# Kernel optimization log

Measured on AMD Instinct MI355X. Metric: run time of the kernel, lower is better.

The kernel has to match this reference:

```python
import jax, jax.numpy as jnp
import numpy as np

B, S, D_H, D_L, K, K_H, W = 4, 4096, 1024, 256, 64, 4, 9


def setup_inputs() -> dict:
    key = jax.random.key(0)
    ks = jax.random.split(key, 6)
    return {
        "inputs": jax.random.normal(ks[0], (B, S, D_H), jnp.float32),
        "W1": jax.random.normal(ks[1], (D_H, D_L), jnp.float32) * 0.02,
        "b1": jnp.zeros((D_L,), jnp.float32),
        "RME": jax.random.normal(ks[2], (D_L, K), jnp.float32),
        "K2": jax.random.normal(ks[3], (K_H, D_L, D_L), jnp.float32) * 0.02,
        "b2": jnp.zeros((D_L,), jnp.float32),
        "Wu": jax.random.normal(ks[4], (D_L, D_H), jnp.float32) * 0.02,
        "bu": jnp.zeros((D_H,), jnp.float32),
        "gamma": jnp.ones((D_H,), jnp.float32),
        "beta": jnp.zeros((D_H,), jnp.float32),
    }


def _memory_reorg(act, RMVs, k_h):
    # act: [B,S,d_l], RMVs: [B,S,k]
    R = jnp.transpose(RMVs, (0, 2, 1))  # [B,k,S]
    h_vars = jnp.mean((R - jnp.mean(R, axis=-1, keepdims=True)) ** 2, axis=-1)  # [B,k]
    top = jnp.argsort(-h_vars, axis=-1)[:, :k_h]                   # [B,k_h]
    h_max = jnp.take_along_axis(R, top[:, :, None], axis=1)        # [B,k_h,S]
    perm = jnp.argsort(h_max, axis=-1)                             # [B,k_h,S] permutation indices
    g = jnp.take_along_axis(act[:, None], perm[..., None], axis=2) # [B,k_h,S,d_l]
    return jnp.transpose(g, (0, 2, 1, 3))                          # [B,S,k_h,d_l]


def reference(inputs, W1, b1, RME, K2, b2, Wu, bu, gamma, beta):
    # DOWN_PROJECTION_1
    q = jax.nn.relu(jnp.einsum('bsh,hd->bsd', inputs, W1) + b1)    # [B,S,d_l]
    # RANDOM_PROJECTION
    RMVs = jnp.einsum('bsd,dk->bsk', q, RME)                       # [B,S,k]
    # Memory reorganization (variance-based argsort permutations)
    qp = _memory_reorg(q, RMVs, K_H)                               # [B,S,k_h,d_l]
    # DOWN_PROJECTION_2
    q2 = jax.nn.relu(jnp.einsum('bskd,kde->bse', qp, K2) + b2)     # [B,S,d_l]
    # Sliding-window key construction (edge windows replicated)
    half = (W - 1) // 2
    widx = jnp.arange(S - W + 1)[:, None] + jnp.arange(W)[None, :]  # [S-W+1, W]
    win = q2[:, widx]                                               # [B,S-W+1,W,d_l]
    first = jnp.broadcast_to(q2[:, None, :W], (B, half, W, D_L))
    last = jnp.broadcast_to(q2[:, None, S - W:], (B, half, W, D_L))
    keyt = jnp.concatenate([first, win, last], axis=1)              # [B,S,W,d_l]
    # Windowed attention
    f = jnp.sqrt(jnp.float32(D_L))
    scores = jax.nn.softmax(jnp.einsum('bsd,bswd->bsw', q2, keyt) / f, axis=-1)  # [B,S,W]
    # UP_PROJECTION on keys -> values
    val = jax.nn.relu(jnp.einsum('bswd,dh->bswh', keyt, Wu) + bu)   # [B,S,W,d_h]
    out = jnp.einsum('bswh,bsw->bsh', val, scores)                  # [B,S,d_h]
    # LayerNorm (keras default epsilon=1e-3) on residual
    x = out + inputs
    mu = jnp.mean(x, axis=-1, keepdims=True)
    var = jnp.mean((x - mu) ** 2, axis=-1, keepdims=True)
    return gamma * (x - mu) * jax.lax.rsqrt(var + 1e-3) + beta
```

## Files before the change

### kernel.cpp

```cpp
#include <hip/hip_runtime.h>

#define B_  4
#define S_  4096
#define DH  1024
#define DL  256
#define KK  64
#define KH  4
#define WW  9

typedef unsigned short ushort_t;
typedef _Float16 f16;
typedef _Float16 f16x8 __attribute__((ext_vector_type(8)));
typedef float  f32x4  __attribute__((ext_vector_type(4)));

__device__ __forceinline__ void gld_lds16(const void* g, void* lds_uniform_base) {
    __builtin_amdgcn_global_load_lds(
        (const __attribute__((address_space(1))) unsigned int*)g,
        (__attribute__((address_space(3))) unsigned int*)lds_uniform_base,
        16, 0, 0);
}

template<bool AFP32, bool GATHER, int OUTMODE>
__global__ __launch_bounds__(256)
void mfma_gemm2(const float* __restrict__ Af,
                const ushort_t* __restrict__ Ah, const ushort_t* __restrict__ Al,
                const ushort_t* __restrict__ Bh, const ushort_t* __restrict__ Bl,
                const float* __restrict__ bias, float* __restrict__ C,
                ushort_t* __restrict__ Ch, ushort_t* __restrict__ Cl,
                const int* __restrict__ gidx, int K, int N, int nbx)
{
    __shared__ __align__(16) ushort_t Abuf[64 * 64 * 2];
    __shared__ __align__(16) ushort_t Bsh[128 * 64];
    __shared__ __align__(16) ushort_t Bsl[128 * 64];

    const int tid = threadIdx.x;
    const int w = tid >> 6, l = tid & 63;
    const int wm = w >> 1, wn = w & 1;
    const int lr = l & 15, lk = l >> 4;
    const int cpx = gridDim.x >> 3;
    const int orig = (blockIdx.x & 7) * cpx + (blockIdx.x >> 3);
    const int m0 = (orig / nbx) * 64, n0 = (orig % nbx) * 128;

    f32x4 acc0[2][4] = {};
    f32x4 acc1[2][4] = {};

    for (int k0 = 0; k0 < K; k0 += 64) {
        if (AFP32) {
            float* Asf = (float*)Abuf;
            #pragma unroll
            for (int it = 0; it < 4; ++it) {
                const int c = it * 256 + tid;
                const int r = c >> 4, cc = c & 15;
                const int cs = cc ^ ((r & 7) << 1);
                const float* src = Af + (size_t)(m0 + r) * K + k0 + cs * 4;
                gld_lds16(src, &Asf[(size_t)c * 4]);
            }
        } else {
            ushort_t* Ash = Abuf;
            ushort_t* Asl = Abuf + 64 * 64;
            #pragma unroll
            for (int it = 0; it < 2; ++it) {
                const int c = it * 256 + tid;
                const int r = c >> 3, kp = c & 7;
                const int kl = kp ^ (r & 7);
                size_t off;
                if (GATHER) {
                    const int rg = gidx[(m0 + r) * KH + (k0 >> 8)];
                    off = (size_t)rg * DL + (k0 & (DL - 1)) + kl * 8;
                } else {
                    off = (size_t)(m0 + r) * K + k0 + kl * 8;
                }
                gld_lds16(Ah + off, &Ash[(size_t)c * 8]);
                gld_lds16(Al + off, &Asl[(size_t)c * 8]);
            }
        }
        #pragma unroll
        for (int it = 0; it < 4; ++it) {
            const int c = it * 256 + tid;
            const int r = c >> 3, kp = c & 7;
            const int kl = kp ^ (r & 7);
            const size_t off = (size_t)(n0 + r) * K + k0 + kl * 8;
            gld_lds16(Bh + off, &Bsh[(size_t)c * 8]);
            gld_lds16(Bl + off, &Bsl[(size_t)c * 8]);
        }
        __syncthreads();

        #pragma unroll
        for (int ks = 0; ks < 2; ++ks) {
            f16x8 ah[2], al[2];
            #pragma unroll
            for (int mf = 0; mf < 2; ++mf) {
                const int row = wm * 32 + mf * 16 + lr;
                const int kb  = ks * 4 + lk;
                if (AFP32) {
                    const float* Asf = (const float*)Abuf;
                    const int fo = row * 64 + ((kb ^ (row & 7)) << 3);
                    const f32x4 lo = *(const f32x4*)&Asf[fo];
                    const f32x4 hi = *(const f32x4*)&Asf[fo + 4];
                    const float xs[8] = {lo[0], lo[1], lo[2], lo[3],
                                         hi[0], hi[1], hi[2], hi[3]};
                    #pragma unroll
                    for (int e = 0; e < 8; ++e) {
                        const f16 h = (f16)xs[e];
                        const f16 lv = (f16)((xs[e] - (float)h) * 2048.0f);
                        ah[mf][e] = h;
                        al[mf][e] = lv;
                    }
                } else {
                    const ushort_t* Ash = Abuf;
                    const ushort_t* Asl = Abuf + 64 * 64;
                    const int o = row * 64 + ((kb ^ (row & 7)) << 3);
                    ah[mf] = *(const f16x8*)&Ash[o];
                    al[mf] = *(const f16x8*)&Asl[o];
                }
            }
            #pragma unroll
            for (int nf = 0; nf < 4; ++nf) {
                const int row = wn * 64 + nf * 16 + lr;
                const int kb  = ks * 4 + lk;
                const int o   = row * 64 + ((kb ^ (row & 7)) << 3);
                const f16x8 bh = *(const f16x8*)&Bsh[o];
                const f16x8 bl = *(const f16x8*)&Bsl[o];
                #pragma unroll
                for (int mf = 0; mf < 2; ++mf) {
                    acc0[mf][nf] = __builtin_amdgcn_mfma_f32_16x16x32_f16(
                        ah[mf], bh, acc0[mf][nf], 0, 0, 0);
                    acc1[mf][nf] = __builtin_amdgcn_mfma_f32_16x16x32_f16(
                        ah[mf], bl, acc1[mf][nf], 0, 0, 0);
                    acc1[mf][nf] = __builtin_amdgcn_mfma_f32_16x16x32_f16(
                        al[mf], bh, acc1[mf][nf], 0, 0, 0);
                }
            }
        }
        __syncthreads();
    }

    float bv[4];
    #pragma unroll
    for (int nf = 0; nf < 4; ++nf)
        bv[nf] = bias[n0 + wn * 64 + nf * 16 + lr];
    #pragma unroll
    for (int mf = 0; mf < 2; ++mf)
        #pragma unroll
        for (int nf = 0; nf < 4; ++nf)
            #pragma unroll
            for (int r = 0; r < 4; ++r) {
                const int m = m0 + wm * 32 + mf * 16 + lk * 4 + r;
                const int n = n0 + wn * 64 + nf * 16 + lr;
                float x = acc0[mf][nf][r] + acc1[mf][nf][r] * (1.0f / 2048.0f) + bv[nf];
                x = fmaxf(x, 0.f);
                C[(size_t)m * N + n] = x;
                if (OUTMODE == 1) {
                    const f16 h = (f16)x;
                    const f16 lo = (f16)((x - (float)h) * 2048.0f);
                    Ch[(size_t)m * N + n] = __builtin_bit_cast(ushort_t, h);
                    Cl[(size_t)m * N + n] = __builtin_bit_cast(ushort_t, lo);
                }
            }
}

__global__ __launch_bounds__(512)
void mfma_gemm_big(const ushort_t* __restrict__ Ah, const ushort_t* __restrict__ Al,
                   const ushort_t* __restrict__ Bh, const ushort_t* __restrict__ Bl,
                   const float* __restrict__ bias, ushort_t* __restrict__ Ch,
                   int K, int N, int nbx)
{
    __shared__ __align__(16) ushort_t Ash[128 * 64];
    __shared__ __align__(16) ushort_t Asl[128 * 64];
    __shared__ __align__(16) ushort_t Bsh[128 * 64];
    __shared__ __align__(16) ushort_t Bsl[128 * 64];

    const int tid = threadIdx.x;
    const int w = tid >> 6, l = tid & 63;
    const int wm = w >> 1, wn = w & 1;
    const int lr = l & 15, lk = l >> 4;
    const int cpx = gridDim.x >> 3;
    const int orig = (blockIdx.x & 7) * cpx + (blockIdx.x >> 3);
    const int m0 = (orig / nbx) * 128, n0 = (orig % nbx) * 128;

    f32x4 acc0[2][4] = {};
    f32x4 acc1[2][4] = {};

    for (int k0 = 0; k0 < K; k0 += 64) {
        #pragma unroll
        for (int it = 0; it < 2; ++it) {
            const int c = it * 512 + tid;
            const int r = c >> 3, kp = c & 7;
            const int kl = kp ^ (r & 7);
            const size_t offA = (size_t)(m0 + r) * K + k0 + kl * 8;
            const size_t offB = (size_t)(n0 + r) * K + k0 + kl * 8;
            gld_lds16(Ah + offA, &Ash[(size_t)c * 8]);
            gld_lds16(Al + offA, &Asl[(size_t)c * 8]);
            gld_lds16(Bh + offB, &Bsh[(size_t)c * 8]);
            gld_lds16(Bl + offB, &Bsl[(size_t)c * 8]);
        }
        __syncthreads();

        #pragma unroll
        for (int ks = 0; ks < 2; ++ks) {
            f16x8 ah[2], al[2];
            #pragma unroll
            for (int mf = 0; mf < 2; ++mf) {
                const int row = wm * 32 + mf * 16 + lr;
                const int kb  = ks * 4 + lk;
                const int o   = row * 64 + ((kb ^ (row & 7)) << 3);
                ah[mf] = *(const f16x8*)&Ash[o];
                al[mf] = *(const f16x8*)&Asl[o];
            }
            #pragma unroll
            for (int nf = 0; nf < 4; ++nf) {
                const int row = wn * 64 + nf * 16 + lr;
                const int kb  = ks * 4 + lk;
                const int o   = row * 64 + ((kb ^ (row & 7)) << 3);
                const f16x8 bh = *(const f16x8*)&Bsh[o];
                const f16x8 bl = *(const f16x8*)&Bsl[o];
                #pragma unroll
                for (int mf = 0; mf < 2; ++mf) {
                    acc0[mf][nf] = __builtin_amdgcn_mfma_f32_16x16x32_f16(
                        ah[mf], bh, acc0[mf][nf], 0, 0, 0);
                    acc1[mf][nf] = __builtin_amdgcn_mfma_f32_16x16x32_f16(
                        ah[mf], bl, acc1[mf][nf], 0, 0, 0);
                    acc1[mf][nf] = __builtin_amdgcn_mfma_f32_16x16x32_f16(
                        al[mf], bh, acc1[mf][nf], 0, 0, 0);
                }
            }
        }
        __syncthreads();
    }

    float bv[4];
    #pragma unroll
    for (int nf = 0; nf < 4; ++nf)
        bv[nf] = bias[n0 + wn * 64 + nf * 16 + lr];
    #pragma unroll
    for (int mf = 0; mf < 2; ++mf)
        #pragma unroll
        for (int nf = 0; nf < 4; ++nf)
            #pragma unroll
            for (int r = 0; r < 4; ++r) {
                const int m = m0 + wm * 32 + mf * 16 + lk * 4 + r;
                const int n = n0 + wn * 64 + nf * 16 + lr;
                float x = acc0[mf][nf][r] + acc1[mf][nf][r] * (1.0f / 2048.0f) + bv[nf];
                x = fmaxf(x, 0.f);
                const f16 hcv = (f16)x;
                Ch[(size_t)m * N + n] = __builtin_bit_cast(ushort_t, hcv);
            }
}

__global__ __launch_bounds__(256)
void tsplit2_kernel(const float* __restrict__ in, ushort_t* __restrict__ t0,
                    ushort_t* __restrict__ t1, int K, int N)
{
    __shared__ float tile[32][33];
    const int t = threadIdx.x;
    const int bk = blockIdx.x * 32, bn = blockIdx.y * 32;
    const int c = t & 31, rb = t >> 5;
    #pragma unroll
    for (int i = 0; i < 4; ++i) {
        const int r = rb + i * 8;
        tile[r][c] = in[(size_t)(bk + r) * N + bn + c];
    }
    __syncthreads();
    #pragma unroll
    for (int i = 0; i < 4; ++i) {
        const int rr = rb + i * 8;
        const float x = tile[c][rr];
        const f16 hv = (f16)x;
        const f16 lv = (f16)((x - (float)hv) * 2048.0f);
        const size_t o = (size_t)(bn + rr) * K + bk + c;
        t0[o] = __builtin_bit_cast(ushort_t, hv);
        t1[o] = __builtin_bit_cast(ushort_t, lv);
    }
}

__global__ __launch_bounds__(256)
void gemm_trans_kernel(const float* __restrict__ A, const float* __restrict__ Bm,
                       float* __restrict__ C, int M, int KA, int N)
{
    constexpr int BK = 16;
    __shared__ float Asb[BK][64 + 4];
    __shared__ float Bsb[BK][64 + 4];
    const int tid = threadIdx.x;
    const int tx = tid & 15, ty = tid >> 4;
    const int m0 = blockIdx.y * 64, n0 = blockIdx.x * 64;

    float acc[4][4] = {};
    const int lr = tid >> 2, lc = (tid & 3) << 2;
    const int kr = tid >> 4, nc = (tid & 15) << 2;

    for (int k0 = 0; k0 < KA; k0 += BK) {
        const float4 a4 = *reinterpret_cast<const float4*>(A + (size_t)(m0 + lr) * KA + k0 + lc);
        const float4 b4 = *reinterpret_cast<const float4*>(Bm + (size_t)(k0 + kr) * N + n0 + nc);
        Asb[lc + 0][lr] = a4.x; Asb[lc + 1][lr] = a4.y;
        Asb[lc + 2][lr] = a4.z; Asb[lc + 3][lr] = a4.w;
        *reinterpret_cast<float4*>(&Bsb[kr][nc]) = b4;
        __syncthreads();
        #pragma unroll
        for (int kk = 0; kk < BK; ++kk) {
            const float4 av = *reinterpret_cast<const float4*>(&Asb[kk][ty << 2]);
            const float4 bv = *reinterpret_cast<const float4*>(&Bsb[kk][tx << 2]);
            const float a[4] = {av.x, av.y, av.z, av.w};
            const float b[4] = {bv.x, bv.y, bv.z, bv.w};
            #pragma unroll
            for (int i = 0; i < 4; ++i)
                #pragma unroll
                for (int j = 0; j < 4; ++j)
                    acc[i][j] = fmaf(a[i], b[j], acc[i][j]);
        }
        __syncthreads();
    }
    #pragma unroll
    for (int i = 0; i < 4; ++i) {
        const int m = m0 + (ty << 2) + i;
        const int b = m >> 12, s = m & (S_ - 1);
        #pragma unroll
        for (int j = 0; j < 4; ++j) {
            const int n = n0 + (tx << 2) + j;
            C[(size_t)(b * N + n) * S_ + s] = acc[i][j];
        }
    }
}

__global__ __launch_bounds__(256)
void var_kernel(const float* __restrict__ rmvT, float* __restrict__ hvars)
{
    const int bk = blockIdx.x;
    const float* src = rmvT + (size_t)bk * S_;
    float s1 = 0.f, s2 = 0.f;
    for (int t = threadIdx.x; t < S_; t += 256) {
        const float v = src[t];
        s1 += v; s2 += v * v;
    }
    #pragma unroll
    for (int off = 32; off; off >>= 1) {
        s1 += __shfl_xor(s1, off);
        s2 += __shfl_xor(s2, off);
    }
    __shared__ float r1[4], r2[4];
    const int wave = threadIdx.x >> 6, lane = threadIdx.x & 63;
    if (lane == 0) { r1[wave] = s1; r2[wave] = s2; }
    __syncthreads();
    if (threadIdx.x == 0) {
        const float t1 = r1[0] + r1[1] + r1[2] + r1[3];
        const float t2 = r2[0] + r2[1] + r2[2] + r2[3];
        const float mu = t1 / (float)S_;
        hvars[bk] = t2 / (float)S_ - mu * mu;
    }
}

__global__ void topk_kernel(const float* __restrict__ hvars, int* __restrict__ topidx)
{
    const int b = threadIdx.x;
    if (b >= B_) return;
    float v[KK];
    for (int k = 0; k < KK; ++k) v[k] = hvars[b * KK + k];
    for (int i = 0; i < KH; ++i) {
        int best = 0; float bv = -3.4e38f;
        for (int k = 0; k < KK; ++k)
            if (v[k] > bv) { bv = v[k]; best = k; }
        topidx[b * KH + i] = best;
        v[best] = -3.4e38f;
    }
}

__global__ __launch_bounds__(256)
void rank_kernel(const float* __restrict__ rmvT, const int* __restrict__ topidx,
                 int* __restrict__ gidx)
{
    const int bi = blockIdx.x;
    const int b = bi >> 2, ih = bi & 3;
    const int k = topidx[b * KH + ih];
    const float* src = rmvT + (size_t)(b * KK + k) * S_;
    __shared__ __align__(16) unsigned long long keys[S_];
    __shared__ int partial[4][64];
    for (int t = threadIdx.x; t < S_; t += 256) {
        const unsigned bits = __builtin_bit_cast(unsigned, src[t]);
        const unsigned u = (bits & 0x80000000u) ? ~bits : (bits | 0x80000000u);
        keys[t] = ((unsigned long long)u << 12) | (unsigned)t;
    }
    __syncthreads();

    const int il = threadIdx.x & 63;
    const int chunk = threadIdx.x >> 6;
    const int i = blockIdx.y * 64 + il;
    const unsigned long long ki = keys[i];

    int cnt = 0;
    const int jbase = chunk << 10;
    #pragma unroll 8
    for (int jj = 0; jj < 1024; jj += 2) {
        const ulonglong2 k2 = *reinterpret_cast<const ulonglong2*>(&keys[jbase + jj]);
        cnt += (int)(k2.x < ki);
        cnt += (int)(k2.y < ki);
    }
    partial[chunk][il] = cnt;
    __syncthreads();
    if (threadIdx.x < 64) {
        const int rank = partial[0][threadIdx.x] + partial[1][threadIdx.x]
                       + partial[2][threadIdx.x] + partial[3][threadIdx.x];
        const int ii = blockIdx.y * 64 + threadIdx.x;
        gidx[((b << 12) + rank) * KH + ih] = (b << 12) + ii;
    }
}

__global__ __launch_bounds__(256)
void final_kernel(const ushort_t* __restrict__ vh, const float* __restrict__ q2,
                  const float* __restrict__ inputs, const float* __restrict__ gamma,
                  const float* __restrict__ beta, float* __restrict__ out)
{
    const int bid = blockIdx.x;
    const int m0 = (((bid & 7) << 9) | (bid >> 3)) << 2;
    const int wave = threadIdx.x >> 6, lane = threadIdx.x & 63;
    const int m = m0 + wave;
    const int s = m & (S_ - 1), b = m >> 12;
    const int jb = (s < 4) ? 0 : (s >= S_ - 4 ? S_ - WW : s - 4);

    const ushort_t* vb = vh + (size_t)(b * S_ + jb) * DH;
    const float* inp = inputs + (size_t)m * DH;
    f16x8 varr[2][WW];
    float4 iv[2][2];
    #pragma unroll
    for (int c = 0; c < 2; ++c) {
        const int h = (c << 9) + (lane << 3);
        #pragma unroll
        for (int w = 0; w < WW; ++w)
            varr[c][w] = *reinterpret_cast<const f16x8*>(vb + (size_t)w * DH + h);
        iv[c][0] = *reinterpret_cast<const float4*>(inp + h);
        iv[c][1] = *reinterpret_cast<const float4*>(inp + h + 4);
    }

    const float4 qv = *reinterpret_cast<const float4*>(q2 + (size_t)m * DL + (lane << 2));
    const float* kbase = q2 + (size_t)(b * S_ + jb) * DL;
    float sc[WW];
    #pragma unroll
    for (int w = 0; w < WW; ++w) {
        const float4 kv = *reinterpret_cast<const float4*>(kbase + w * DL + (lane << 2));
        float d = qv.x * kv.x + qv.y * kv.y + qv.z * kv.z + qv.w * kv.w;
        #pragma unroll
        for (int off = 32; off; off >>= 1) d += __shfl_xor(d, off);
        sc[w] = d * 0.0625f;
    }
    float mx = sc[0];
    #pragma unroll
    for (int w = 1; w < WW; ++w) mx = fmaxf(mx, sc[w]);
    float wgt[WW]; float sum = 0.f;
    #pragma unroll
    for (int w = 0; w < WW; ++w) { wgt[w] = __expf(sc[w] - mx); sum += wgt[w]; }
    const float inv = 1.f / sum;
    #pragma unroll
    for (int w = 0; w < WW; ++w) wgt[w] *= inv;

    float x[2][8];
    float s1 = 0.f, s2 = 0.f;
    #pragma unroll
    for (int c = 0; c < 2; ++c) {
        float acc[8] = {};
        #pragma unroll
        for (int w = 0; w < WW; ++w) {
            const f16x8 vv = varr[c][w];
            #pragma unroll
            for (int e = 0; e < 8; ++e)
                acc[e] = fmaf(wgt[w], (float)vv[e], acc[e]);
        }
        #pragma unroll
        for (int e = 0; e < 8; ++e) {
            const float ivv = (e < 4) ? (&iv[c][0].x)[e] : (&iv[c][1].x)[e - 4];
            acc[e] += ivv;
            x[c][e] = acc[e];
            s1 += acc[e];
            s2 += acc[e] * acc[e];
        }
    }

    #pragma unroll
    for (int off = 32; off; off >>= 1) {
        s1 += __shfl_xor(s1, off);
        s2 += __shfl_xor(s2, off);
    }
    const float mu = s1 / (float)DH;
    const float rs = rsqrtf(s2 / (float)DH - mu * mu + 0.001f);

    #pragma unroll
    for (int c = 0; c < 2; ++c) {
        const int h = (c << 9) + (lane << 3);
        #pragma unroll
        for (int half = 0; half < 2; ++half) {
            const float4 g  = *reinterpret_cast<const float4*>(gamma + h + half * 4);
            const float4 bt = *reinterpret_cast<const float4*>(beta + h + half * 4);
            float4 o;
            o.x = g.x * (x[c][half * 4 + 0] - mu) * rs + bt.x;
            o.y = g.y * (x[c][half * 4 + 1] - mu) * rs + bt.y;
            o.z = g.z * (x[c][half * 4 + 2] - mu) * rs + bt.z;
            o.w = g.w * (x[c][half * 4 + 3] - mu) * rs + bt.w;
            *reinterpret_cast<float4*>(out + (size_t)m * DH + h + half * 4) = o;
        }
    }
}

extern "C" void kernel_launch(void* const* d_in, const int* in_sizes, int n_in,
                              void* d_out, int out_size, void* d_ws, size_t ws_size,
                              hipStream_t stream)
{
    (void)in_sizes; (void)n_in; (void)out_size; (void)ws_size;
    const float* inputs = (const float*)d_in[0];
    const float* W1     = (const float*)d_in[1];
    const float* b1     = (const float*)d_in[2];
    const float* RME    = (const float*)d_in[3];
    const float* K2     = (const float*)d_in[4];
    const float* b2     = (const float*)d_in[5];
    const float* Wu     = (const float*)d_in[6];
    const float* bu     = (const float*)d_in[7];
    const float* gamma  = (const float*)d_in[8];
    const float* beta   = (const float*)d_in[9];
    float* out = (float*)d_out;

    char* ws = (char*)d_ws;
    const size_t MB = 1u << 20;
    ushort_t* vh  = (ushort_t*)(ws + 0 * MB);
    float*    q   = (float*)   (ws + 64 * MB);
    ushort_t* qh  = (ushort_t*)(ws + 80 * MB);
    ushort_t* ql  = (ushort_t*)(ws + 88 * MB);
    float*    q2  = (float*)   (ws + 96 * MB);
    ushort_t* q2h = (ushort_t*)(ws + 112 * MB);
    ushort_t* q2l = (ushort_t*)(ws + 120 * MB);
    float*    rmvT= (float*)   (ws + 128 * MB);
    float*    hvars  = (float*)(ws + 132 * MB);
    int*      topidx = (int*)  (ws + 132 * MB + 4096);
    int*      gidx   = (int*)  (ws + 132 * MB + 8192);
    ushort_t* w1th = (ushort_t*)(ws + 133 * MB);
    ushort_t* w1tl = w1th + (DH * DL);
    ushort_t* k2th = w1tl + (DH * DL);
    ushort_t* k2tl = k2th + (KH * DL * DL);
    ushort_t* wuth = k2tl + (KH * DL * DL);
    ushort_t* wutl = wuth + (DL * DH);

    const int M = B_ * S_;

    tsplit2_kernel<<<dim3(DH / 32, DL / 32), dim3(256), 0, stream>>>(W1, w1th, w1tl, DH, DL);
    tsplit2_kernel<<<dim3(KH * DL / 32, DL / 32), dim3(256), 0, stream>>>((const float*)K2, k2th, k2tl, KH * DL, DL);
    tsplit2_kernel<<<dim3(DL / 32, DH / 32), dim3(256), 0, stream>>>(Wu, wuth, wutl, DL, DH);

    mfma_gemm2<true, false, 1><<<dim3((DL / 128) * (M / 64)), dim3(256), 0, stream>>>(
        inputs, nullptr, nullptr, w1th, w1tl, b1, q, qh, ql, nullptr, DH, DL, DL / 128);
    gemm_trans_kernel<<<dim3(KK / 64, M / 64), dim3(256), 0, stream>>>(q, RME, rmvT, M, DL, KK);
    var_kernel<<<dim3(B_ * KK), dim3(256), 0, stream>>>(rmvT, hvars);
    topk_kernel<<<dim3(1), dim3(64), 0, stream>>>(hvars, topidx);
    rank_kernel<<<dim3(B_ * KH, S_ / 64), dim3(256), 0, stream>>>(rmvT, topidx, gidx);
    mfma_gemm2<false, true, 1><<<dim3((DL / 128) * (M / 64)), dim3(256), 0, stream>>>(
        nullptr, qh, ql, k2th, k2tl, b2, q2, q2h, q2l, gidx, KH * DL, DL, DL / 128);
    mfma_gemm_big<<<dim3((DH / 128) * (M / 128)), dim3(512), 0, stream>>>(
        q2h, q2l, wuth, wutl, bu, vh, DL, DH, DH / 128);
    final_kernel<<<dim3(M / 4), dim3(256), 0, stream>>>(vh, q2, inputs, gamma, beta, out);
}
```

Measured before the change: 191.9 us.

## Use single-f16 up-projection GEMM and shrink small GEMM tiles to 64x64

```diff
diff --git a/kernel.cpp b/kernel.cpp
--- a/kernel.cpp
+++ b/kernel.cpp
@@ -20,18 +20,18 @@
         16, 0, 0);
 }
 
-template<bool AFP32, bool GATHER, int OUTMODE>
+template<bool AFP32, bool GATHER, bool WL>
 __global__ __launch_bounds__(256)
-void mfma_gemm2(const float* __restrict__ Af,
-                const ushort_t* __restrict__ Ah, const ushort_t* __restrict__ Al,
-                const ushort_t* __restrict__ Bh, const ushort_t* __restrict__ Bl,
-                const float* __restrict__ bias, float* __restrict__ C,
-                ushort_t* __restrict__ Ch, ushort_t* __restrict__ Cl,
-                const int* __restrict__ gidx, int K, int N, int nbx)
+void mfma_gemm_sm(const float* __restrict__ Af,
+                  const ushort_t* __restrict__ Ah, const ushort_t* __restrict__ Al,
+                  const ushort_t* __restrict__ Bh, const ushort_t* __restrict__ Bl,
+                  const float* __restrict__ bias, float* __restrict__ C,
+                  ushort_t* __restrict__ Ch, ushort_t* __restrict__ Cl,
+                  const int* __restrict__ gidx, int K, int N, int nbx)
 {
     __shared__ __align__(16) ushort_t Abuf[64 * 64 * 2];
-    __shared__ __align__(16) ushort_t Bsh[128 * 64];
-    __shared__ __align__(16) ushort_t Bsl[128 * 64];
+    __shared__ __align__(16) ushort_t Bsh[64 * 64];
+    __shared__ __align__(16) ushort_t Bsl[64 * 64];
 
     const int tid = threadIdx.x;
     const int w = tid >> 6, l = tid & 63;
@@ -39,10 +39,10 @@
     const int lr = l & 15, lk = l >> 4;
     const int cpx = gridDim.x >> 3;
     const int orig = (blockIdx.x & 7) * cpx + (blockIdx.x >> 3);
-    const int m0 = (orig / nbx) * 64, n0 = (orig % nbx) * 128;
-
-    f32x4 acc0[2][4] = {};
-    f32x4 acc1[2][4] = {};
+    const int m0 = (orig / nbx) * 64, n0 = (orig % nbx) * 64;
+
+    f32x4 acc0[2][2] = {};
+    f32x4 acc1[2][2] = {};
 
     for (int k0 = 0; k0 < K; k0 += 64) {
         if (AFP32) {
@@ -63,19 +63,19 @@
                 const int c = it * 256 + tid;
                 const int r = c >> 3, kp = c & 7;
                 const int kl = kp ^ (r & 7);
-                size_t off;
+                size_t offA;
                 if (GATHER) {
                     const int rg = gidx[(m0 + r) * KH + (k0 >> 8)];
-                    off = (size_t)rg * DL + (k0 & (DL - 1)) + kl * 8;
+                    offA = (size_t)rg * DL + (k0 & (DL - 1)) + kl * 8;
                 } else {
-                    off = (size_t)(m0 + r) * K + k0 + kl * 8;
+                    offA = (size_t)(m0 + r) * K + k0 + kl * 8;
                 }
-                gld_lds16(Ah + off, &Ash[(size_t)c * 8]);
-                gld_lds16(Al + off, &Asl[(size_t)c * 8]);
-            }
-        }
-        #pragma unroll
-        for (int it = 0; it < 4; ++it) {
+                gld_lds16(Ah + offA, &Ash[(size_t)c * 8]);
+                gld_lds16(Al + offA, &Asl[(size_t)c * 8]);
+            }
+        }
+        #pragma unroll
+        for (int it = 0; it < 2; ++it) {
             const int c = it * 256 + tid;
             const int r = c >> 3, kp = c & 7;
             const int kl = kp ^ (r & 7);
@@ -115,8 +115,8 @@
                 }
             }
             #pragma unroll
-            for (int nf = 0; nf < 4; ++nf) {
-                const int row = wn * 64 + nf * 16 + lr;
+            for (int nf = 0; nf < 2; ++nf) {
+                const int row = wn * 32 + nf * 16 + lr;
                 const int kb  = ks * 4 + lk;
                 const int o   = row * 64 + ((kb ^ (row & 7)) << 3);
                 const f16x8 bh = *(const f16x8*)&Bsh[o];
@@ -135,40 +135,37 @@
         __syncthreads();
     }
 
-    float bv[4];
-    #pragma unroll
-    for (int nf = 0; nf < 4; ++nf)
-        bv[nf] = bias[n0 + wn * 64 + nf * 16 + lr];
+    float bv[2];
+    #pragma unroll
+    for (int nf = 0; nf < 2; ++nf)
+        bv[nf] = bias[n0 + wn * 32 + nf * 16 + lr];
     #pragma unroll
     for (int mf = 0; mf < 2; ++mf)
         #pragma unroll
-        for (int nf = 0; nf < 4; ++nf)
+        for (int nf = 0; nf < 2; ++nf)
             #pragma unroll
             for (int r = 0; r < 4; ++r) {
                 const int m = m0 + wm * 32 + mf * 16 + lk * 4 + r;
-                const int n = n0 + wn * 64 + nf * 16 + lr;
+                const int n = n0 + wn * 32 + nf * 16 + lr;
                 float x = acc0[mf][nf][r] + acc1[mf][nf][r] * (1.0f / 2048.0f) + bv[nf];
                 x = fmaxf(x, 0.f);
                 C[(size_t)m * N + n] = x;
-                if (OUTMODE == 1) {
-                    const f16 h = (f16)x;
+                const f16 h = (f16)x;
+                Ch[(size_t)m * N + n] = __builtin_bit_cast(ushort_t, h);
+                if (WL) {
                     const f16 lo = (f16)((x - (float)h) * 2048.0f);
-                    Ch[(size_t)m * N + n] = __builtin_bit_cast(ushort_t, h);
                     Cl[(size_t)m * N + n] = __builtin_bit_cast(ushort_t, lo);
                 }
             }
 }
 
 __global__ __launch_bounds__(512)
-void mfma_gemm_big(const ushort_t* __restrict__ Ah, const ushort_t* __restrict__ Al,
-                   const ushort_t* __restrict__ Bh, const ushort_t* __restrict__ Bl,
-                   const float* __restrict__ bias, ushort_t* __restrict__ Ch,
-                   int K, int N, int nbx)
+void mfma_gemm1l(const ushort_t* __restrict__ Ah, const ushort_t* __restrict__ Bh,
+                 const float* __restrict__ bias, ushort_t* __restrict__ Ch,
+                 int K, int N, int nbx)
 {
     __shared__ __align__(16) ushort_t Ash[128 * 64];
-    __shared__ __align__(16) ushort_t Asl[128 * 64];
     __shared__ __align__(16) ushort_t Bsh[128 * 64];
-    __shared__ __align__(16) ushort_t Bsl[128 * 64];
 
     const int tid = threadIdx.x;
     const int w = tid >> 6, l = tid & 63;
@@ -179,7 +176,6 @@
     const int m0 = (orig / nbx) * 128, n0 = (orig % nbx) * 128;
 
     f32x4 acc0[2][4] = {};
-    f32x4 acc1[2][4] = {};
 
     for (int k0 = 0; k0 < K; k0 += 64) {
         #pragma unroll
@@ -190,39 +186,28 @@
             const size_t offA = (size_t)(m0 + r) * K + k0 + kl * 8;
             const size_t offB = (size_t)(n0 + r) * K + k0 + kl * 8;
             gld_lds16(Ah + offA, &Ash[(size_t)c * 8]);
-            gld_lds16(Al + offA, &Asl[(size_t)c * 8]);
             gld_lds16(Bh + offB, &Bsh[(size_t)c * 8]);
-            gld_lds16(Bl + offB, &Bsl[(size_t)c * 8]);
         }
         __syncthreads();
 
         #pragma unroll
         for (int ks = 0; ks < 2; ++ks) {
-            f16x8 ah[2], al[2];
+            f16x8 ah[2];
             #pragma unroll
             for (int mf = 0; mf < 2; ++mf) {
                 const int row = wm * 32 + mf * 16 + lr;
                 const int kb  = ks * 4 + lk;
-                const int o   = row * 64 + ((kb ^ (row & 7)) << 3);
-                ah[mf] = *(const f16x8*)&Ash[o];
-                al[mf] = *(const f16x8*)&Asl[o];
+                ah[mf] = *(const f16x8*)&Ash[row * 64 + ((kb ^ (row & 7)) << 3)];
             }
             #pragma unroll
             for (int nf = 0; nf < 4; ++nf) {
                 const int row = wn * 64 + nf * 16 + lr;
                 const int kb  = ks * 4 + lk;
-                const int o   = row * 64 + ((kb ^ (row & 7)) << 3);
-                const f16x8 bh = *(const f16x8*)&Bsh[o];
-                const f16x8 bl = *(const f16x8*)&Bsl[o];
+                const f16x8 bh = *(const f16x8*)&Bsh[row * 64 + ((kb ^ (row & 7)) << 3)];
                 #pragma unroll
-                for (int mf = 0; mf < 2; ++mf) {
+                for (int mf = 0; mf < 2; ++mf)
                     acc0[mf][nf] = __builtin_amdgcn_mfma_f32_16x16x32_f16(
                         ah[mf], bh, acc0[mf][nf], 0, 0, 0);
-                    acc1[mf][nf] = __builtin_amdgcn_mfma_f32_16x16x32_f16(
-                        ah[mf], bl, acc1[mf][nf], 0, 0, 0);
-                    acc1[mf][nf] = __builtin_amdgcn_mfma_f32_16x16x32_f16(
-                        al[mf], bh, acc1[mf][nf], 0, 0, 0);
-                }
             }
         }
         __syncthreads();
@@ -240,7 +225,7 @@
             for (int r = 0; r < 4; ++r) {
                 const int m = m0 + wm * 32 + mf * 16 + lk * 4 + r;
                 const int n = n0 + wn * 64 + nf * 16 + lr;
-                float x = acc0[mf][nf][r] + acc1[mf][nf][r] * (1.0f / 2048.0f) + bv[nf];
+                float x = acc0[mf][nf][r] + bv[nf];
                 x = fmaxf(x, 0.f);
                 const f16 hcv = (f16)x;
                 Ch[(size_t)m * N + n] = __builtin_bit_cast(ushort_t, hcv);
@@ -522,7 +507,6 @@
     ushort_t* ql  = (ushort_t*)(ws + 88 * MB);
     float*    q2  = (float*)   (ws + 96 * MB);
     ushort_t* q2h = (ushort_t*)(ws + 112 * MB);
-    ushort_t* q2l = (ushort_t*)(ws + 120 * MB);
     float*    rmvT= (float*)   (ws + 128 * MB);
     float*    hvars  = (float*)(ws + 132 * MB);
     int*      topidx = (int*)  (ws + 132 * MB + 4096);
@@ -540,15 +524,15 @@
     tsplit2_kernel<<<dim3(KH * DL / 32, DL / 32), dim3(256), 0, stream>>>((const float*)K2, k2th, k2tl, KH * DL, DL);
     tsplit2_kernel<<<dim3(DL / 32, DH / 32), dim3(256), 0, stream>>>(Wu, wuth, wutl, DL, DH);
 
-    mfma_gemm2<true, false, 1><<<dim3((DL / 128) * (M / 64)), dim3(256), 0, stream>>>(
-        inputs, nullptr, nullptr, w1th, w1tl, b1, q, qh, ql, nullptr, DH, DL, DL / 128);
+    mfma_gemm_sm<true, false, true><<<dim3((DL / 64) * (M / 64)), dim3(256), 0, stream>>>(
+        inputs, nullptr, nullptr, w1th, w1tl, b1, q, qh, ql, nullptr, DH, DL, DL / 64);
     gemm_trans_kernel<<<dim3(KK / 64, M / 64), dim3(256), 0, stream>>>(q, RME, rmvT, M, DL, KK);
     var_kernel<<<dim3(B_ * KK), dim3(256), 0, stream>>>(rmvT, hvars);
     topk_kernel<<<dim3(1), dim3(64), 0, stream>>>(hvars, topidx);
     rank_kernel<<<dim3(B_ * KH, S_ / 64), dim3(256), 0, stream>>>(rmvT, topidx, gidx);
-    mfma_gemm2<false, true, 1><<<dim3((DL / 128) * (M / 64)), dim3(256), 0, stream>>>(
-        nullptr, qh, ql, k2th, k2tl, b2, q2, q2h, q2l, gidx, KH * DL, DL, DL / 128);
-    mfma_gemm_big<<<dim3((DH / 128) * (M / 128)), dim3(512), 0, stream>>>(
-        q2h, q2l, wuth, wutl, bu, vh, DL, DH, DH / 128);
+    mfma_gemm_sm<false, true, false><<<dim3((DL / 64) * (M / 64)), dim3(256), 0, stream>>>(
+        nullptr, qh, ql, k2th, k2tl, b2, q2, q2h, nullptr, gidx, KH * DL, DL, DL / 64);
+    mfma_gemm1l<<<dim3((DH / 128) * (M / 128)), dim3(512), 0, stream>>>(
+        q2h, wuth, bu, vh, DL, DH, DH / 128);
     final_kernel<<<dim3(M / 4), dim3(256), 0, stream>>>(vh, q2, inputs, gamma, beta, out);
 }
```

Measured after the change: 189.2 us. Within noise of the previous version (-1.4%).
